# Kernel tuning notes

Measured on AMD Instinct MI355X. Metric: run time of the kernel, lower is better.

## Reference

```python
import jax, jax.numpy as jnp
import numpy as np

TOP_K = 4

def setup_inputs() -> dict:
    key = jax.random.key(0)
    ks = jax.random.split(key, 10)
    s = 0.02
    return {
        "x": jax.random.normal(ks[0], (4, 1024, 2048), jnp.float32),
        "expert_bias": jnp.zeros((64,), jnp.float32),
        "router_w": jax.random.normal(ks[1], (64, 2048), jnp.float32) * s,
        "gate_w": jax.random.normal(ks[2], (8192, 2048), jnp.float32) * s,
        "up_w": jax.random.normal(ks[3], (8192, 2048), jnp.float32) * s,
        "down_w": jax.random.normal(ks[4], (2048, 8192), jnp.float32) * s,
        "w_down": jax.random.normal(ks[5], (512, 2048), jnp.float32) * s,
        "w_up": jax.random.normal(ks[6], (2048, 512), jnp.float32) * s,
        "experts_w12": jax.random.normal(ks[7], (64, 512, 2048), jnp.float32) * s,
        "experts_w3": jax.random.normal(ks[8], (64, 1024, 512), jnp.float32) * s,
    }


def reference(x, expert_bias, router_w, gate_w, up_w, down_w, w_down, w_up, experts_w12, experts_w3):
    B, S, D = x.shape
    E = router_w.shape[0]
    K = TOP_K
    h = x.reshape(-1, D)            # [N, D]
    N = h.shape[0]
    NK = N * K

    # --- router (fp32) ---
    logits = h @ router_w.T          # [N, E]
    scores = jax.nn.sigmoid(logits)
    z_loss = jnp.mean(logits * logits) * 1e-4
    sel = scores + expert_bias
    _, topk_idx = jax.lax.top_k(sel, K)                      # [N, K]
    topk_logits = jnp.take_along_axis(logits, topk_idx, axis=1)
    gating = jax.nn.softmax(topk_logits, axis=-1)            # [N, K]

    # --- shared SwiGLU expert ---
    shared = (jax.nn.silu(h @ gate_w.T) * (h @ up_w.T)) @ down_w.T   # [N, D]

    # --- bottleneck down projection ---
    hd = h @ w_down.T                # [N, bottle]
    Bn = hd.shape[1]

    # --- dispatch: sort tokens by expert, capacity max_load per expert ---
    flat = topk_idx.reshape(-1)                      # [NK]
    perm = jnp.argsort(flat)                         # stable sort
    sorted_e = flat[perm]
    counts = jnp.bincount(flat, length=E)
    ptr = jnp.cumsum(counts) - counts                # start offset per expert
    local = jnp.arange(NK) - ptr[sorted_e]           # rank within expert
    max_load = (NK // E // 8 + 6) * 8                # static python int
    num_slots = E * max_load
    mask = local < max_load
    slots = sorted_e * max_load + local
    tok = jnp.repeat(jnp.arange(N), K)               # token id per routed slot

    # reverse_map[slot] = token index (N = dummy)
    rm = jnp.full((num_slots + 1,), N, dtype=jnp.int32)
    rm = rm.at[jnp.where(mask, slots, num_slots)].set(tok[perm].astype(jnp.int32))
    reverse_map = rm[:num_slots]

    hwd = jnp.concatenate([hd, jnp.zeros((1, Bn), hd.dtype)], axis=0)
    padding = hwd[reverse_map].reshape(E, max_load, Bn)

    # --- grouped expert GEMMs ---
    h12 = jnp.einsum('emb,ebf->emf', padding, experts_w12)   # [E, L, 2*F]
    h1, h2 = jnp.split(h12, 2, axis=-1)
    pout = jnp.einsum('emf,efb->emb', jax.nn.silu(h1) * h2, experts_w3)
    pout = pout.reshape(-1, Bn)                              # [num_slots, bottle]

    # --- combine: gather back per (token, k) slot and mix with gating ---
    powd = jnp.concatenate([pout, jnp.zeros((1, Bn), pout.dtype)], axis=0)
    gm = jnp.full((NK + 1,), num_slots, dtype=jnp.int32)
    gm = gm.at[jnp.where(mask, perm, NK)].set(jnp.where(mask, slots, num_slots).astype(jnp.int32))
    gather_map = gm[:NK]
    gathered = powd[gather_map].reshape(N, K, Bn)
    routed_b = jnp.einsum('nk,nkb->nb', gating, gathered)
    routed = routed_b @ w_up.T                               # [N, D]

    # eval mode: route_scale = 1.0, moe_scale = 0.5 (one shared expert), aux_loss = 0
    out = (shared + routed) * 0.5
    return out.reshape(B, S, D), z_loss
```

## Files before the change

kernel.cpp:

```cpp
#include <hip/hip_runtime.h>
#include <math.h>

#define NTOK 4096
#define DMODEL 2048
#define ENUM 64
#define HSH 8192
#define BND 512
#define FEXP 1024
#define MAXL 304
#define EPAD 384
#define ECH 16

typedef float f32x4 __attribute__((ext_vector_type(4)));
using bf16x8 = __attribute__((ext_vector_type(8))) __bf16;

typedef const __attribute__((address_space(1))) unsigned int cgu32;
typedef __attribute__((address_space(3))) unsigned int lu32;
#define GLOAD16(g, l) __builtin_amdgcn_global_load_lds((cgu32*)(g), (lu32*)(l), 16, 0, 0)

__device__ __forceinline__ unsigned short f2bf(float f) {
    union { float f; unsigned int u; } v; v.f = f;
    unsigned int u = v.u;
    return (unsigned short)((u + 0x7FFFu + ((u >> 16) & 1u)) >> 16);
}
__device__ __forceinline__ float bf2f(unsigned short s) {
    union { unsigned int u; float f; } v; v.u = ((unsigned int)s) << 16;
    return v.f;
}

__global__ __launch_bounds__(256) void init_kernel(float* zacc, int* slot2tok, unsigned short* hdz) {
    int i = blockIdx.x * 256 + threadIdx.x;
    if (i == 0) *zacc = 0.f;
    if (i < ENUM * MAXL) slot2tok[i] = NTOK;
    if (i < BND) hdz[i] = 0;
}

__global__ __launch_bounds__(256) void convert_kernel(
    const float* __restrict__ in, unsigned short* __restrict__ out, long long n)
{
    long long stride = (long long)gridDim.x * 256 * 8;
    for (long long i = ((long long)blockIdx.x * 256 + threadIdx.x) * 8; i < n; i += stride) {
        float4 a = *(const float4*)(in + i);
        float4 b = *(const float4*)(in + i + 4);
        union { unsigned short s[8]; uint4 v; } o;
        o.s[0] = f2bf(a.x); o.s[1] = f2bf(a.y); o.s[2] = f2bf(a.z); o.s[3] = f2bf(a.w);
        o.s[4] = f2bf(b.x); o.s[5] = f2bf(b.y); o.s[6] = f2bf(b.z); o.s[7] = f2bf(b.w);
        *(uint4*)(out + i) = o.v;
    }
}

__global__ __launch_bounds__(256) void convert_x_kernel(
    const float* __restrict__ in, unsigned short* __restrict__ hi,
    unsigned short* __restrict__ lo, long long n)
{
    long long stride = (long long)gridDim.x * 256 * 8;
    for (long long i = ((long long)blockIdx.x * 256 + threadIdx.x) * 8; i < n; i += stride) {
        float4 a = *(const float4*)(in + i);
        float4 b = *(const float4*)(in + i + 4);
        union { unsigned short s[8]; uint4 v; } oh, ol;
        float f[8] = {a.x, a.y, a.z, a.w, b.x, b.y, b.z, b.w};
#pragma unroll
        for (int j = 0; j < 8; j++) {
            unsigned short h = f2bf(f[j]);
            oh.s[j] = h;
            ol.s[j] = f2bf(f[j] - bf2f(h));
        }
        *(uint4*)(hi + i) = oh.v;
        *(uint4*)(lo + i) = ol.v;
    }
}

__global__ __launch_bounds__(256) void convert_rw_kernel(
    const float* __restrict__ rw, unsigned short* __restrict__ whi,
    unsigned short* __restrict__ wlo)
{
    int i = (blockIdx.x * 256 + threadIdx.x) * 4;
    if (i >= 128 * 2048) return;
    ushort4 oh = {0, 0, 0, 0}, ol = {0, 0, 0, 0};
    if (i < 64 * 2048) {
        float4 f = *(const float4*)(rw + i);
        float v[4] = {f.x, f.y, f.z, f.w};
        unsigned short h;
        h = f2bf(v[0]); oh.x = h; ol.x = f2bf(v[0] - bf2f(h));
        h = f2bf(v[1]); oh.y = h; ol.y = f2bf(v[1] - bf2f(h));
        h = f2bf(v[2]); oh.z = h; ol.z = f2bf(v[2] - bf2f(h));
        h = f2bf(v[3]); oh.w = h; ol.w = f2bf(v[3] - bf2f(h));
    }
    *(ushort4*)(whi + i) = oh;
    *(ushort4*)(wlo + i) = ol;
}

__global__ __launch_bounds__(256) void tconv_kernel(
    const float* __restrict__ in, unsigned short* __restrict__ out, int Kd, int Nd)
{
    __shared__ float t[32][33];
    size_t zoff = (size_t)blockIdx.z * Kd * Nd;
    in += zoff; out += zoff;
    int n0 = blockIdx.x * 32, k0 = blockIdx.y * 32;
    int r = threadIdx.x >> 3, c = (threadIdx.x & 7) * 4;
    float4 v = *(const float4*)(in + (size_t)(k0 + r) * Nd + n0 + c);
    t[r][c] = v.x; t[r][c + 1] = v.y; t[r][c + 2] = v.z; t[r][c + 3] = v.w;
    __syncthreads();
    ushort4 o;
    o.x = f2bf(t[c + 0][r]); o.y = f2bf(t[c + 1][r]);
    o.z = f2bf(t[c + 2][r]); o.w = f2bf(t[c + 3][r]);
    *(ushort4*)(out + (size_t)(n0 + r) * Kd + k0 + c) = o;
}

__global__ __launch_bounds__(256) void rgemm_kernel(
    const unsigned short* __restrict__ xb, const unsigned short* __restrict__ xlo,
    const unsigned short* __restrict__ whi, const unsigned short* __restrict__ wlo,
    float* __restrict__ logits)
{
    __shared__ unsigned short As[2][128 * 64];
    __shared__ unsigned short Bs[2][128 * 64];
    const int z = blockIdx.z;
    const int m0 = blockIdx.y * 128;
    const int tid = threadIdx.x;
    const int lane = tid & 63;
    const int w = tid >> 6;
    const int wm = (w >> 1) * 64;
    const int wn = (w & 1) * 64;

    const unsigned short* Ab = (z == 2) ? xlo : xb;
    const unsigned short* Bb = (z == 1) ? wlo : whi;
    float* Cb = logits + (size_t)z * NTOK * 128;

    size_t asrc[4], bsrc[4];
    int ldso[4];
#pragma unroll
    for (int i = 0; i < 4; i++) {
        int u = i * 256 + tid;
        int r = u >> 3;
        int ce = ((u & 7) ^ (r & 7)) * 8;
        ldso[i] = u * 8;
        asrc[i] = (size_t)(m0 + r) * DMODEL + ce;
        bsrc[i] = (size_t)r * DMODEL + ce;
    }

    const int lrow = lane & 15;
    const int kg = lane >> 4;
    const int mk = (lrow & 7) << 4;
    int arx[4], brx[4];
#pragma unroll
    for (int t = 0; t < 4; t++) {
        arx[t] = (wm + t * 16 + lrow) * 128;
        brx[t] = (wn + t * 16 + lrow) * 128;
    }

    f32x4 acc[4][4];
#pragma unroll
    for (int a = 0; a < 4; a++)
#pragma unroll
        for (int b = 0; b < 4; b++) acc[a][b] = (f32x4)0.f;

#pragma unroll
    for (int i = 0; i < 4; i++) GLOAD16(Ab + asrc[i], &As[0][ldso[i]]);
#pragma unroll
    for (int i = 0; i < 4; i++) GLOAD16(Bb + bsrc[i], &Bs[0][ldso[i]]);
    __syncthreads();

    int cur = 0;
    for (int k0 = 0; k0 < DMODEL; k0 += 64) {
        const int kn = k0 + 64;
        if (kn < DMODEL) {
            const int nxt = cur ^ 1;
#pragma unroll
            for (int i = 0; i < 4; i++) GLOAD16(Ab + asrc[i] + kn, &As[nxt][ldso[i]]);
#pragma unroll
            for (int i = 0; i < 4; i++) GLOAD16(Bb + bsrc[i] + kn, &Bs[nxt][ldso[i]]);
        }
        const char* Abase = (const char*)&As[cur][0];
        const char* Bbase = (const char*)&Bs[cur][0];
#pragma unroll
        for (int ks = 0; ks < 2; ks++) {
            const int cb = (ks * 64 + kg * 16) ^ mk;
            bf16x8 a[4], b[4];
#pragma unroll
            for (int t = 0; t < 4; t++) {
                a[t] = *(const bf16x8*)(Abase + arx[t] + cb);
                b[t] = *(const bf16x8*)(Bbase + brx[t] + cb);
            }
#pragma unroll
            for (int ni = 0; ni < 4; ni++)
#pragma unroll
                for (int mi = 0; mi < 4; mi++)
                    acc[mi][ni] = __builtin_amdgcn_mfma_f32_16x16x32_bf16(a[mi], b[ni], acc[mi][ni], 0, 0, 0);
        }
        __syncthreads();
        cur ^= 1;
    }

    const int rb0 = m0 + wm + (kg << 2);
#pragma unroll
    for (int mi = 0; mi < 4; mi++)
#pragma unroll
        for (int ni = 0; ni < 4; ni++) {
            int col = wn + ni * 16 + lrow;
#pragma unroll
            for (int r = 0; r < 4; r++)
                Cb[(size_t)(rb0 + mi * 16 + r) * 128 + col] = acc[mi][ni][r];
        }
}

__global__ __launch_bounds__(256) void topk_kernel(
    const float* __restrict__ logits, const float* __restrict__ bias,
    int* __restrict__ topk_idx, float* __restrict__ gating, float* __restrict__ zacc)
{
    __shared__ float zpart[4];
    const size_t Z = (size_t)NTOK * 128;
    int wv = threadIdx.x >> 6, lane = threadIdx.x & 63;
    int n = blockIdx.x * 4 + wv;
    const float* lp = logits + (size_t)n * 128 + lane;
    float logit = lp[0] + lp[Z] + lp[2 * Z];
    float sel = 1.f / (1.f + expf(-logit)) + bias[lane];
    float zsq = logit * logit;
    for (int off = 32; off; off >>= 1) zsq += __shfl_down(zsq, off);
    if (lane == 0) zpart[wv] = zsq;
    __syncthreads();
    if (threadIdx.x == 0) atomicAdd(zacc, zpart[0] + zpart[1] + zpart[2] + zpart[3]);
    float cur = sel;
    float ch_logit[4]; int ch_idx[4];
    for (int kk = 0; kk < 4; kk++) {
        float v = cur; int idx = lane;
        for (int off = 1; off < 64; off <<= 1) {
            float v2 = __shfl_xor(v, off);
            int i2 = __shfl_xor(idx, off);
            if (v2 > v || (v2 == v && i2 < idx)) { v = v2; idx = i2; }
        }
        ch_idx[kk] = idx;
        ch_logit[kk] = __shfl(logit, idx);
        if (lane == idx) cur = -1e30f;
    }
    if (lane == 0) {
        float mx = ch_logit[0];
        for (int kk = 1; kk < 4; kk++) mx = fmaxf(mx, ch_logit[kk]);
        float se = 0.f, ex[4];
        for (int kk = 0; kk < 4; kk++) { ex[kk] = expf(ch_logit[kk] - mx); se += ex[kk]; }
        for (int kk = 0; kk < 4; kk++) {
            topk_idx[n * 4 + kk] = ch_idx[kk];
            gating[n * 4 + kk] = ex[kk] / se;
        }
    }
}

__global__ __launch_bounds__(256) void rank_kernel(
    const int* __restrict__ topk_idx, int* __restrict__ slot2tok, int* __restrict__ gmap)
{
    int e = blockIdx.x;
    __shared__ int wsum[4];
    int tid = threadIdx.x;
    int lane = tid & 63, w = tid >> 6;
    int running = 0;
    for (int c = 0; c < NTOK * 4; c += 256) {
        int i = c + tid;
        int fl = topk_idx[i];
        bool m = (fl == e);
        unsigned long long bal = __ballot(m);
        int prefix = __popcll(bal & ((1ULL << lane) - 1ULL));
        if (lane == 0) wsum[w] = __popcll(bal);
        __syncthreads();
        int wbase = 0;
        for (int j = 0; j < w; j++) wbase += wsum[j];
        int total = wsum[0] + wsum[1] + wsum[2] + wsum[3];
        if (m) {
            int rank = running + wbase + prefix;
            int tok = i >> 2;
            if (rank < MAXL) {
                slot2tok[e * MAXL + rank] = tok;
                gmap[i] = e * MAXL + rank;
            } else gmap[i] = -1;
        }
        running += total;
        __syncthreads();
    }
}

template<int GATHER, int EPI>
__global__ __launch_bounds__(256) void gemm2(
    const unsigned short* __restrict__ A, long long aZ, int lda,
    const int* __restrict__ gtab,
    const unsigned short* __restrict__ Bm, long long bZ, int ldb,
    void* __restrict__ Cb, long long cZ, int ldc,
    int M, int K)
{
    __shared__ unsigned short As[2][128 * 64];
    __shared__ unsigned short Bs[2][128 * 64];
    const int z = blockIdx.z;
    const int m0 = blockIdx.y * 128;
    const int n0 = blockIdx.x * 128;
    const int tid = threadIdx.x;
    const int lane = tid & 63;
    const int w = tid >> 6;
    const int wm = (w >> 1) * 64;
    const int wn = (w & 1) * 64;

    const unsigned short* Ab = A + (GATHER ? (size_t)0 : (size_t)z * aZ);
    const unsigned short* Bb = Bm + (size_t)z * bZ;

    size_t asrc[4], bsrc[4];
    int ldso[4];
#pragma unroll
    for (int i = 0; i < 4; i++) {
        int u = i * 256 + tid;
        int r = u >> 3;
        int ce = ((u & 7) ^ (r & 7)) * 8;
        ldso[i] = u * 8;
        if constexpr (GATHER) {
            int mr = m0 + r;
            int tok = (mr < M) ? gtab[(size_t)z * MAXL + mr] : NTOK;
            asrc[i] = (size_t)tok * lda + ce;
        } else {
            asrc[i] = (size_t)(m0 + r) * lda + ce;
        }
        bsrc[i] = (size_t)(n0 + r) * ldb + ce;
    }

    const int lrow = lane & 15;
    const int kg = lane >> 4;
    const int mk = (lrow & 7) << 4;
    int arx[4], brx[4];
#pragma unroll
    for (int t = 0; t < 4; t++) {
        arx[t] = (wm + t * 16 + lrow) * 128;
        brx[t] = (wn + t * 16 + lrow) * 128;
    }

    f32x4 acc[4][4];
#pragma unroll
    for (int a = 0; a < 4; a++)
#pragma unroll
        for (int b = 0; b < 4; b++) acc[a][b] = (f32x4)0.f;

#pragma unroll
    for (int i = 0; i < 4; i++) GLOAD16(Ab + asrc[i], &As[0][ldso[i]]);
#pragma unroll
    for (int i = 0; i < 4; i++) GLOAD16(Bb + bsrc[i], &Bs[0][ldso[i]]);
    __syncthreads();

    int cur = 0;
    for (int k0 = 0; k0 < K; k0 += 64) {
        const int kn = k0 + 64;
        if (kn < K) {
            const int nxt = cur ^ 1;
#pragma unroll
            for (int i = 0; i < 4; i++) GLOAD16(Ab + asrc[i] + kn, &As[nxt][ldso[i]]);
#pragma unroll
            for (int i = 0; i < 4; i++) GLOAD16(Bb + bsrc[i] + kn, &Bs[nxt][ldso[i]]);
        }
        const char* Abase = (const char*)&As[cur][0];
        const char* Bbase = (const char*)&Bs[cur][0];
#pragma unroll
        for (int ks = 0; ks < 2; ks++) {
            const int cb = (ks * 64 + kg * 16) ^ mk;
            bf16x8 a[4], b[4];
#pragma unroll
            for (int t = 0; t < 4; t++) {
                a[t] = *(const bf16x8*)(Abase + arx[t] + cb);
                b[t] = *(const bf16x8*)(Bbase + brx[t] + cb);
            }
#pragma unroll
            for (int ni = 0; ni < 4; ni++)
#pragma unroll
                for (int mi = 0; mi < 4; mi++)
                    acc[mi][ni] = __builtin_amdgcn_mfma_f32_16x16x32_bf16(a[mi], b[ni], acc[mi][ni], 0, 0, 0);
        }
        __syncthreads();
        cur ^= 1;
    }

    const int rb0 = m0 + wm + (kg << 2);
#pragma unroll
    for (int mi = 0; mi < 4; mi++)
#pragma unroll
        for (int ni = 0; ni < 4; ni++) {
            int col = n0 + wn + ni * 16 + lrow;
#pragma unroll
            for (int r = 0; r < 4; r++) {
                int row = rb0 + mi * 16 + r;
                if (row < M) {
                    size_t ci = (size_t)z * cZ + (size_t)row * ldc + col;
                    float v = acc[mi][ni][r];
                    if constexpr (EPI == 0) {
                        ((unsigned short*)Cb)[ci] = f2bf(v);
                    } else if constexpr (EPI == 1) {
                        unsigned short* cp = (unsigned short*)Cb + ci;
                        float g = bf2f(*cp);
                        *cp = f2bf(g / (1.f + expf(-g)) * v);
                    } else if constexpr (EPI == 2) {
                        ((float*)Cb)[ci] = v;
                    } else {
                        float* cp = (float*)Cb + ci;
                        *cp = (*cp + v) * 0.5f;
                    }
                }
            }
        }
}

__global__ __launch_bounds__(256) void siluact_kernel(
    const unsigned short* __restrict__ h12, unsigned short* __restrict__ act)
{
    int e = blockIdx.y, m = blockIdx.x;
    const unsigned short* hr = h12 + ((size_t)e * EPAD + m) * 2048;
    unsigned short* ar = act + ((size_t)e * EPAD + m) * 1024;
    int j = threadIdx.x * 4;
    ushort4 h1 = *(const ushort4*)(hr + j);
    ushort4 h2 = *(const ushort4*)(hr + 1024 + j);
    ushort4 o;
    float v;
    v = bf2f(h1.x); o.x = f2bf(v / (1.f + expf(-v)) * bf2f(h2.x));
    v = bf2f(h1.y); o.y = f2bf(v / (1.f + expf(-v)) * bf2f(h2.y));
    v = bf2f(h1.z); o.z = f2bf(v / (1.f + expf(-v)) * bf2f(h2.z));
    v = bf2f(h1.w); o.w = f2bf(v / (1.f + expf(-v)) * bf2f(h2.w));
    *(ushort4*)(ar + j) = o;
}

__global__ __launch_bounds__(256) void gather_kernel(
    const unsigned short* __restrict__ pout, const int* __restrict__ gmap,
    const float* __restrict__ gating, unsigned short* __restrict__ routed_b)
{
    int n = blockIdx.x;
    int j = threadIdx.x * 2;
    float a0 = 0.f, a1 = 0.f;
#pragma unroll
    for (int kk = 0; kk < 4; kk++) {
        int slot = gmap[n * 4 + kk];
        float g = gating[n * 4 + kk];
        if (slot >= 0) {
            const unsigned short* pr = pout + (size_t)slot * BND + j;
            a0 += g * bf2f(pr[0]);
            a1 += g * bf2f(pr[1]);
        }
    }
    routed_b[(size_t)n * BND + j] = f2bf(a0);
    routed_b[(size_t)n * BND + j + 1] = f2bf(a1);
}

__global__ void zloss_kernel(const float* zacc, float* out) {
    out[0] = zacc[0] * (1.0e-4f / (float)(NTOK * ENUM));
}

extern "C" void kernel_launch(void* const* d_in, const int* in_sizes, int n_in,
                              void* d_out, int out_size, void* d_ws, size_t ws_size,
                              hipStream_t stream)
{
    const float* x      = (const float*)d_in[0];
    const float* ebias  = (const float*)d_in[1];
    const float* rw     = (const float*)d_in[2];
    const float* gate_w = (const float*)d_in[3];
    const float* up_w   = (const float*)d_in[4];
    const float* down_w = (const float*)d_in[5];
    const float* w_down = (const float*)d_in[6];
    const float* w_up   = (const float*)d_in[7];
    const float* w12    = (const float*)d_in[8];
    const float* w3     = (const float*)d_in[9];
    float* out = (float*)d_out;

    char* ws = (char*)d_ws;
    size_t off = 0;
    auto alloc = [&](size_t b) { size_t o = off; off += (b + 255) & ~(size_t)255; return o; };
    float* zacc     = (float*)(ws + alloc(4));
    int*   topk     = (int*)(ws + alloc((size_t)NTOK * 4 * 4));
    float* gating   = (float*)(ws + alloc((size_t)NTOK * 4 * 4));
    int*   gmap     = (int*)(ws + alloc((size_t)NTOK * 4 * 4));
    int*   slot2tok = (int*)(ws + alloc((size_t)ENUM * MAXL * 4));
    unsigned short* xb     = (unsigned short*)(ws + alloc((size_t)NTOK * DMODEL * 2));
    unsigned short* hd     = (unsigned short*)(ws + alloc((size_t)(NTOK + 1) * BND * 2));
    unsigned short* rb     = (unsigned short*)(ws + alloc((size_t)NTOK * BND * 2));
    unsigned short* wdownb = (unsigned short*)(ws + alloc((size_t)BND * DMODEL * 2));
    unsigned short* wupb   = (unsigned short*)(ws + alloc((size_t)DMODEL * BND * 2));
    unsigned short* wbuf   = (unsigned short*)(ws + alloc((size_t)HSH * DMODEL * 2));
    unsigned short* H1     = (unsigned short*)(ws + alloc((size_t)NTOK * HSH * 2));
    unsigned short* h12  = H1;
    unsigned short* act  = H1 + (size_t)ECH * EPAD * 2048;
    unsigned short* pout = H1 + (size_t)ECH * EPAD * 2048 + (size_t)ECH * EPAD * 1024;
    unsigned short* xlo    = H1;
    float*          logits = (float*)((char*)H1 + (size_t)NTOK * DMODEL * 2);
    unsigned short* whi    = (unsigned short*)((char*)logits + (size_t)3 * NTOK * 128 * 4);
    unsigned short* wlo    = whi + (size_t)128 * DMODEL;

    init_kernel<<<(ENUM * MAXL + 255) / 256, 256, 0, stream>>>(zacc, slot2tok, hd + (size_t)NTOK * BND);

    convert_x_kernel<<<1024, 256, 0, stream>>>(x, xb, xlo, (long long)NTOK * DMODEL);
    convert_rw_kernel<<<(128 * 2048 / 4 + 255) / 256, 256, 0, stream>>>(rw, whi, wlo);
    rgemm_kernel<<<dim3(1, NTOK / 128, 3), 256, 0, stream>>>(xb, xlo, whi, wlo, logits);
    topk_kernel<<<NTOK / 4, 256, 0, stream>>>(logits, ebias, topk, gating, zacc);
    rank_kernel<<<ENUM, 256, 0, stream>>>(topk, slot2tok, gmap);

    convert_kernel<<<256, 256, 0, stream>>>(w_down, wdownb, (long long)BND * DMODEL);
    convert_kernel<<<256, 256, 0, stream>>>(w_up, wupb, (long long)DMODEL * BND);

    gemm2<0, 0><<<dim3(BND / 128, NTOK / 128, 1), 256, 0, stream>>>(
        xb, 0, DMODEL, nullptr, wdownb, 0, DMODEL, hd, 0, BND, NTOK, DMODEL);

    convert_kernel<<<1024, 256, 0, stream>>>(gate_w, wbuf, (long long)HSH * DMODEL);
    gemm2<0, 0><<<dim3(HSH / 128, NTOK / 128, 1), 256, 0, stream>>>(
        xb, 0, DMODEL, nullptr, wbuf, 0, DMODEL, H1, 0, HSH, NTOK, DMODEL);
    convert_kernel<<<1024, 256, 0, stream>>>(up_w, wbuf, (long long)HSH * DMODEL);
    gemm2<0, 1><<<dim3(HSH / 128, NTOK / 128, 1), 256, 0, stream>>>(
        xb, 0, DMODEL, nullptr, wbuf, 0, DMODEL, H1, 0, HSH, NTOK, DMODEL);
    convert_kernel<<<1024, 256, 0, stream>>>(down_w, wbuf, (long long)DMODEL * HSH);
    gemm2<0, 2><<<dim3(DMODEL / 128, NTOK / 128, 1), 256, 0, stream>>>(
        H1, 0, HSH, nullptr, wbuf, 0, HSH, out, 0, DMODEL, NTOK, HSH);

    for (int c = 0; c < ENUM / ECH; c++) {
        tconv_kernel<<<dim3(2048 / 32, 512 / 32, ECH), 256, 0, stream>>>(
            w12 + (size_t)c * ECH * 512 * 2048, wbuf, 512, 2048);
        gemm2<1, 0><<<dim3(2048 / 128, 3, ECH), 256, 0, stream>>>(
            hd, 0, BND, slot2tok + (size_t)c * ECH * MAXL,
            wbuf, (long long)2048 * 512, 512,
            h12, (long long)EPAD * 2048, 2048, MAXL, BND);
        tconv_kernel<<<dim3(512 / 32, 1024 / 32, ECH), 256, 0, stream>>>(
            w3 + (size_t)c * ECH * 1024 * 512, wbuf, 1024, 512);
        siluact_kernel<<<dim3(EPAD, ECH), 256, 0, stream>>>(h12, act);
        gemm2<0, 0><<<dim3(BND / 128, 3, ECH), 256, 0, stream>>>(
            act, (long long)EPAD * FEXP, FEXP, nullptr,
            wbuf, (long long)BND * FEXP, FEXP,
            pout + (size_t)c * ECH * MAXL * BND, (long long)MAXL * BND, BND, MAXL, FEXP);
    }

    gather_kernel<<<NTOK, 256, 0, stream>>>(pout, gmap, gating, rb);

    gemm2<0, 3><<<dim3(DMODEL / 128, NTOK / 128, 1), 256, 0, stream>>>(
        rb, 0, BND, nullptr, wupb, 0, BND, out, 0, DMODEL, NTOK, BND);

    zloss_kernel<<<1, 1, 0, stream>>>(zacc, out + (size_t)NTOK * DMODEL);
}
```

Before: 1.112 ms.

## Prefetch two K-tiles ahead with explicit vmcnt waits in GEMM main loops

Both bf16 MFMA GEMM kernels now issue the first two K-tiles up front and, each iteration, wait with s_waitcnt vmcnt(8) so only the current tile's global-to-LDS loads must finish before compute. The next-next tile is then loaded into the buffer just consumed. The goal is to keep more global loads in flight and replace __syncthreads with raw s_barrier plus sched_barrier. The vmcnt count assumes exactly 8 outstanding loads per tile. That holds as written, but it is fragile if the compiler emits any other vector memory ops in the loop.

```diff
diff --git a/kernel.cpp b/kernel.cpp
--- a/kernel.cpp
+++ b/kernel.cpp
@@ -158,18 +158,18 @@
     for (int i = 0; i < 4; i++) GLOAD16(Ab + asrc[i], &As[0][ldso[i]]);
 #pragma unroll
     for (int i = 0; i < 4; i++) GLOAD16(Bb + bsrc[i], &Bs[0][ldso[i]]);
-    __syncthreads();
-
+#pragma unroll
+    for (int i = 0; i < 4; i++) GLOAD16(Ab + asrc[i] + 64, &As[1][ldso[i]]);
+#pragma unroll
+    for (int i = 0; i < 4; i++) GLOAD16(Bb + bsrc[i] + 64, &Bs[1][ldso[i]]);
+
+    const int nt = DMODEL >> 6;
     int cur = 0;
-    for (int k0 = 0; k0 < DMODEL; k0 += 64) {
-        const int kn = k0 + 64;
-        if (kn < DMODEL) {
-            const int nxt = cur ^ 1;
-#pragma unroll
-            for (int i = 0; i < 4; i++) GLOAD16(Ab + asrc[i] + kn, &As[nxt][ldso[i]]);
-#pragma unroll
-            for (int i = 0; i < 4; i++) GLOAD16(Bb + bsrc[i] + kn, &Bs[nxt][ldso[i]]);
-        }
+    for (int t = 0; t < nt; ++t) {
+        if (t + 1 < nt) asm volatile("s_waitcnt vmcnt(8)" ::: "memory");
+        else            asm volatile("s_waitcnt vmcnt(0)" ::: "memory");
+        __builtin_amdgcn_s_barrier();
+        __builtin_amdgcn_sched_barrier(0);
         const char* Abase = (const char*)&As[cur][0];
         const char* Bbase = (const char*)&Bs[cur][0];
 #pragma unroll
@@ -177,9 +177,9 @@
             const int cb = (ks * 64 + kg * 16) ^ mk;
             bf16x8 a[4], b[4];
 #pragma unroll
-            for (int t = 0; t < 4; t++) {
-                a[t] = *(const bf16x8*)(Abase + arx[t] + cb);
-                b[t] = *(const bf16x8*)(Bbase + brx[t] + cb);
+            for (int t2 = 0; t2 < 4; t2++) {
+                a[t2] = *(const bf16x8*)(Abase + arx[t2] + cb);
+                b[t2] = *(const bf16x8*)(Bbase + brx[t2] + cb);
             }
 #pragma unroll
             for (int ni = 0; ni < 4; ni++)
@@ -187,7 +187,17 @@
                 for (int mi = 0; mi < 4; mi++)
                     acc[mi][ni] = __builtin_amdgcn_mfma_f32_16x16x32_bf16(a[mi], b[ni], acc[mi][ni], 0, 0, 0);
         }
-        __syncthreads();
+        __builtin_amdgcn_sched_barrier(0);
+        asm volatile("s_waitcnt lgkmcnt(0)" ::: "memory");
+        __builtin_amdgcn_s_barrier();
+        __builtin_amdgcn_sched_barrier(0);
+        const int kn = (t + 2) * 64;
+        if (kn < DMODEL) {
+#pragma unroll
+            for (int i = 0; i < 4; i++) GLOAD16(Ab + asrc[i] + kn, &As[cur][ldso[i]]);
+#pragma unroll
+            for (int i = 0; i < 4; i++) GLOAD16(Bb + bsrc[i] + kn, &Bs[cur][ldso[i]]);
+        }
         cur ^= 1;
     }
 
@@ -336,18 +346,20 @@
     for (int i = 0; i < 4; i++) GLOAD16(Ab + asrc[i], &As[0][ldso[i]]);
 #pragma unroll
     for (int i = 0; i < 4; i++) GLOAD16(Bb + bsrc[i], &Bs[0][ldso[i]]);
-    __syncthreads();
-
+    if (64 < K) {
+#pragma unroll
+        for (int i = 0; i < 4; i++) GLOAD16(Ab + asrc[i] + 64, &As[1][ldso[i]]);
+#pragma unroll
+        for (int i = 0; i < 4; i++) GLOAD16(Bb + bsrc[i] + 64, &Bs[1][ldso[i]]);
+    }
+
+    const int nt = K >> 6;
     int cur = 0;
-    for (int k0 = 0; k0 < K; k0 += 64) {
-        const int kn = k0 + 64;
-        if (kn < K) {
-            const int nxt = cur ^ 1;
-#pragma unroll
-            for (int i = 0; i < 4; i++) GLOAD16(Ab + asrc[i] + kn, &As[nxt][ldso[i]]);
-#pragma unroll
-            for (int i = 0; i < 4; i++) GLOAD16(Bb + bsrc[i] + kn, &Bs[nxt][ldso[i]]);
-        }
+    for (int t = 0; t < nt; ++t) {
+        if (t + 1 < nt) asm volatile("s_waitcnt vmcnt(8)" ::: "memory");
+        else            asm volatile("s_waitcnt vmcnt(0)" ::: "memory");
+        __builtin_amdgcn_s_barrier();
+        __builtin_amdgcn_sched_barrier(0);
         const char* Abase = (const char*)&As[cur][0];
         const char* Bbase = (const char*)&Bs[cur][0];
 #pragma unroll
@@ -355,9 +367,9 @@
             const int cb = (ks * 64 + kg * 16) ^ mk;
             bf16x8 a[4], b[4];
 #pragma unroll
-            for (int t = 0; t < 4; t++) {
-                a[t] = *(const bf16x8*)(Abase + arx[t] + cb);
-                b[t] = *(const bf16x8*)(Bbase + brx[t] + cb);
+            for (int t2 = 0; t2 < 4; t2++) {
+                a[t2] = *(const bf16x8*)(Abase + arx[t2] + cb);
+                b[t2] = *(const bf16x8*)(Bbase + brx[t2] + cb);
             }
 #pragma unroll
             for (int ni = 0; ni < 4; ni++)
@@ -365,7 +377,17 @@
                 for (int mi = 0; mi < 4; mi++)
                     acc[mi][ni] = __builtin_amdgcn_mfma_f32_16x16x32_bf16(a[mi], b[ni], acc[mi][ni], 0, 0, 0);
         }
-        __syncthreads();
+        __builtin_amdgcn_sched_barrier(0);
+        asm volatile("s_waitcnt lgkmcnt(0)" ::: "memory");
+        __builtin_amdgcn_s_barrier();
+        __builtin_amdgcn_sched_barrier(0);
+        const int kn = (t + 2) * 64;
+        if (kn < K) {
+#pragma unroll
+            for (int i = 0; i < 4; i++) GLOAD16(Ab + asrc[i] + kn, &As[cur][ldso[i]]);
+#pragma unroll
+            for (int i = 0; i < 4; i++) GLOAD16(Bb + bsrc[i] + kn, &Bs[cur][ldso[i]]);
+        }
         cur ^= 1;
     }
 
```

Measured after the change: 1.097 ms. Within noise of the previous version (-1.4%).
